# Kernel optimization log

Hardware: AMD Instinct MI355X
Metric: run time of the kernel (lower is better)

The kernel has to match this reference:

```python
import jax, jax.numpy as jnp
import numpy as np

NEG_SLOPE_ATT = 0.2   # GATConv internal leaky_relu slope
NEG_SLOPE_ACT = 0.01  # f.leaky_relu default
LN_EPS = 1e-5

N_NODES, N_EDGES, F_IN = 50000, 400000, 256
HEADS, C1, C2, N_CLS = 4, 256, 128, 32


def gat_conv(x, src, dst, W, a_src, a_dst, bias, concat):
    """PyG GATConv (self-loops already appended to src/dst)."""
    N = x.shape[0]
    H, C = a_src.shape
    h = (x @ W.T).reshape(N, H, C)                      # [N,H,C]
    s = (h * a_src[None]).sum(-1)                       # [N,H] alpha_src
    d = (h * a_dst[None]).sum(-1)                       # [N,H] alpha_dst
    e = jax.nn.leaky_relu(s[src] + d[dst], NEG_SLOPE_ATT)  # [E,H]
    emax = jax.ops.segment_max(e, dst, num_segments=N)
    emax = jnp.where(jnp.isfinite(emax), emax, 0.0)
    p = jnp.exp(e - emax[dst])
    denom = jax.ops.segment_sum(p, dst, num_segments=N)
    alpha = p / (denom[dst] + 1e-16)                    # segment softmax over dst
    out = jax.ops.segment_sum(alpha[:, :, None] * h[src], dst, num_segments=N)
    out = out.reshape(N, H * C) if concat else out.mean(axis=1)
    return out + bias


def layer_norm(x, g, b):
    mu = x.mean(-1, keepdims=True)
    var = jnp.var(x, axis=-1, keepdims=True)
    return (x - mu) / jnp.sqrt(var + LN_EPS) * g + b


def setup_inputs() -> dict:
    key = jax.random.key(0)
    ks = jax.random.split(key, 24)
    def g(k, shape, scale=0.1):
        return jax.random.normal(k, shape, dtype=jnp.float32) * scale
    inp = {
        "x": g(ks[0], (N_NODES, F_IN), 1.0),
        "edge_src": jax.random.randint(ks[1], (N_EDGES,), 0, N_NODES, dtype=jnp.int32),
        "edge_dst": jax.random.randint(ks[2], (N_EDGES,), 0, N_NODES, dtype=jnp.int32),
        # layer 1: in F_IN -> H*C1 (concat)
        "W1": g(ks[3], (HEADS * C1, F_IN)),
        "a_src1": g(ks[4], (HEADS, C1)), "a_dst1": g(ks[5], (HEADS, C1)),
        "b1": jnp.zeros((HEADS * C1,), jnp.float32),
        "ln1_g": jnp.ones((HEADS * C1,), jnp.float32), "ln1_b": jnp.zeros((HEADS * C1,), jnp.float32),
        # layer 2: in H*C1 -> H*C2 (concat)
        "W2": g(ks[6], (HEADS * C2, HEADS * C1)),
        "a_src2": g(ks[7], (HEADS, C2)), "a_dst2": g(ks[8], (HEADS, C2)),
        "b2": jnp.zeros((HEADS * C2,), jnp.float32),
        "ln2_g": jnp.ones((HEADS * C2,), jnp.float32), "ln2_b": jnp.zeros((HEADS * C2,), jnp.float32),
        # layer 3: in H*C2 -> N_CLS (heads=1, mean/no-concat)
        "W3": g(ks[9], (1 * N_CLS, HEADS * C2)),
        "a_src3": g(ks[10], (1, N_CLS)), "a_dst3": g(ks[11], (1, N_CLS)),
        "b3": jnp.zeros((N_CLS,), jnp.float32),
        "ln3_g": jnp.ones((N_CLS,), jnp.float32), "ln3_b": jnp.zeros((N_CLS,), jnp.float32),
    }
    return inp


def reference(x, edge_src, edge_dst,
              W1, a_src1, a_dst1, b1, ln1_g, ln1_b,
              W2, a_src2, a_dst2, b2, ln2_g, ln2_b,
              W3, a_src3, a_dst3, b3, ln3_g, ln3_b):
    N = x.shape[0]
    loops = jnp.arange(N, dtype=edge_src.dtype)  # GATConv add_self_loops=True
    src = jnp.concatenate([edge_src, loops])
    dst = jnp.concatenate([edge_dst, loops])
    # dropout layers are identity in eval mode
    h = gat_conv(x, src, dst, W1, a_src1, a_dst1, b1, True)
    h = jax.nn.leaky_relu(layer_norm(h, ln1_g, ln1_b), NEG_SLOPE_ACT)
    h = gat_conv(h, src, dst, W2, a_src2, a_dst2, b2, True)
    h = jax.nn.leaky_relu(layer_norm(h, ln2_g, ln2_b), NEG_SLOPE_ACT)
    h = gat_conv(h, src, dst, W3, a_src3, a_dst3, b3, False)
    h = layer_norm(h, ln3_g, ln3_b)
    return jax.nn.log_softmax(h, axis=1)
```

## Files before the change

kernel.cpp:

```cpp
#include <hip/hip_runtime.h>
#include <math.h>


#define NEG_ATT 0.2f
#define NEG_ACT 0.01f

typedef __attribute__((ext_vector_type(8))) short bf16x8;
typedef __attribute__((ext_vector_type(8))) unsigned short u16x8;
typedef __attribute__((ext_vector_type(4))) float f32x4;

__device__ __forceinline__ float bf2f(unsigned short u) {
  union { unsigned int i; float f; } c; c.i = ((unsigned int)u) << 16; return c.f;
}
__device__ __forceinline__ unsigned short f2bf(float f) {
  union { float f; unsigned int i; } c; c.f = f;
  unsigned int r = c.i + 0x7FFFu + ((c.i >> 16) & 1u);
  return (unsigned short)(r >> 16);
}

__global__ void cvt_kernel(const float* __restrict__ in,
                           unsigned short* __restrict__ out, int n8) {
  int i = blockIdx.x * 256 + threadIdx.x;
  if (i >= n8) return;
  float4 v0 = reinterpret_cast<const float4*>(in)[i * 2];
  float4 v1 = reinterpret_cast<const float4*>(in)[i * 2 + 1];
  ushort4 o0 = make_ushort4(f2bf(v0.x), f2bf(v0.y), f2bf(v0.z), f2bf(v0.w));
  ushort4 o1 = make_ushort4(f2bf(v1.x), f2bf(v1.y), f2bf(v1.z), f2bf(v1.w));
  reinterpret_cast<ushort4*>(out)[i * 2] = o0;
  reinterpret_cast<ushort4*>(out)[i * 2 + 1] = o1;
}

__global__ __launch_bounds__(256) void qb_kernel(const float* __restrict__ W1,
    const float* __restrict__ as1, const float* __restrict__ ad1,
    unsigned short* __restrict__ Qb) {
  int r = blockIdx.x;
  int k = threadIdx.x;
  if (r >= 8) { Qb[r * 256 + k] = 0; return; }
  int h = r & 3;
  const float* av = (r >> 2) ? ad1 : as1;
  float acc = 0.f;
#pragma unroll 8
  for (int c = 0; c < 256; c++)
    acc += W1[((size_t)(h * 256 + c)) * 256 + k] * av[h * 256 + c];
  Qb[r * 256 + k] = f2bf(acc);
}

__global__ void hist_kernel(const int* __restrict__ edge_dst,
                            int* __restrict__ cnt, int E, int N) {
  int e = blockIdx.x * 256 + threadIdx.x;
  if (e >= E + N) return;
  int dn = (e < E) ? edge_dst[e] : (e - E);
  atomicAdd(&cnt[dn], 1);
}

__global__ __launch_bounds__(1024) void scan_kernel(const int* __restrict__ cnt,
    int* __restrict__ row_ptr, int* __restrict__ cur, int N) {
  __shared__ int sbuf[1024];
  int tid = threadIdx.x;
  int CH = (N + 1023) / 1024;
  int beg = tid * CH;
  int end = beg + CH; if (end > N) end = N;
  int lsum = 0;
  for (int i = beg; i < end; i++) lsum += cnt[i];
  sbuf[tid] = lsum;
  __syncthreads();
  for (int off = 1; off < 1024; off <<= 1) {
    int v = (tid >= off) ? sbuf[tid - off] : 0;
    __syncthreads();
    sbuf[tid] += v;
    __syncthreads();
  }
  int run = sbuf[tid] - lsum;
  for (int i = beg; i < end; i++) {
    row_ptr[i] = run; cur[i] = run;
    run += cnt[i];
  }
  if (tid == 1023) row_ptr[N] = sbuf[1023];
}

__global__ void scatter_kernel(const int* __restrict__ edge_src,
                               const int* __restrict__ edge_dst,
                               int* __restrict__ cur,
                               int* __restrict__ src_sorted, int E, int N) {
  int e = blockIdx.x * 256 + threadIdx.x;
  if (e >= E + N) return;
  int sn, dn;
  if (e < E) { sn = edge_src[e]; dn = edge_dst[e]; }
  else       { sn = dn = e - E; }
  int pos = atomicAdd(&cur[dn], 1);
  src_sorted[pos] = sn;
}

#define GLOBAL_AS __attribute__((address_space(1)))
#define LDS_AS __attribute__((address_space(3)))

__device__ __forceinline__ void gload_lds16(const void* g, void* l) {
  __builtin_amdgcn_global_load_lds((const GLOBAL_AS unsigned int*)g,
                                   (LDS_AS unsigned int*)l, 16, 0, 0);
}

template <int BM, int BN, int WM, int WN, bool F32OUT>
__global__ __launch_bounds__(256) void gemm_mfma(
    const unsigned short* __restrict__ A, const unsigned short* __restrict__ B,
    void* __restrict__ Cv, const float* __restrict__ bias,
    int M, int N, int K, int lda, int ldb, int ldc,
    long long aZ, long long bZ, long long cZ, int biasZ) {
  constexpr int BK = 64;
  constexpr int FM = BM / (WM * 16);
  constexpr int FN = BN / (WN * 16);
  A += (size_t)blockIdx.z * aZ;
  B += (size_t)blockIdx.z * bZ;
  const size_t cbase = (size_t)blockIdx.z * cZ;
  __shared__ unsigned short As[BM * BK];
  __shared__ unsigned short Bs[BN * BK];
  const int tid = threadIdx.x;
  const int w = tid >> 6, lane = tid & 63;
  const int wm = w / WN, wn = w % WN;
  const int bm = blockIdx.x * BM, bn = blockIdx.y * BN;
  const int l15 = lane & 15, l4 = lane >> 4;

  f32x4 acc[FM][FN] = {};

  constexpr int CHA = BM * BK / 8;
  constexpr int CHB = BN * BK / 8;

  for (int k0 = 0; k0 < K; k0 += BK) {
#pragma unroll
    for (int c0 = 0; c0 < CHA; c0 += 256) {
      int c = c0 + tid;
      if (CHA - c0 >= 256 || tid < CHA - c0) {
        int cl = c ^ ((c >> 3) & 7);
        int row = cl >> 3;
        int kk = (cl & 7) * 8;
        int gr = bm + row; if (gr > M - 1) gr = M - 1;
        gload_lds16(A + (size_t)gr * lda + k0 + kk,
                    As + (size_t)(c0 + (tid & ~63)) * 8);
      }
    }
#pragma unroll
    for (int c0 = 0; c0 < CHB; c0 += 256) {
      int c = c0 + tid;
      if (CHB - c0 >= 256 || tid < CHB - c0) {
        int cl = c ^ ((c >> 3) & 7);
        int row = cl >> 3;
        int kk = (cl & 7) * 8;
        gload_lds16(B + (size_t)(bn + row) * ldb + k0 + kk,
                    Bs + (size_t)(c0 + (tid & ~63)) * 8);
      }
    }
    __syncthreads();
#pragma unroll
    for (int ks = 0; ks < 2; ks++) {
      bf16x8 af[FM], bfr[FN];
#pragma unroll
      for (int i = 0; i < FM; i++) {
        int row = wm * (FM * 16) + i * 16 + l15;
        int byte = row * (BK * 2) + ks * 64 + l4 * 16;
        byte ^= ((byte >> 7) & 7) << 4;
        af[i] = *reinterpret_cast<const bf16x8*>((const char*)As + byte);
      }
#pragma unroll
      for (int i = 0; i < FN; i++) {
        int row = wn * (FN * 16) + i * 16 + l15;
        int byte = row * (BK * 2) + ks * 64 + l4 * 16;
        byte ^= ((byte >> 7) & 7) << 4;
        bfr[i] = *reinterpret_cast<const bf16x8*>((const char*)Bs + byte);
      }
#pragma unroll
      for (int i = 0; i < FM; i++)
#pragma unroll
        for (int jn = 0; jn < FN; jn++)
          acc[i][jn] = __builtin_amdgcn_mfma_f32_16x16x32_bf16(
              af[i], bfr[jn], acc[i][jn], 0, 0, 0);
    }
    __syncthreads();
  }
#pragma unroll
  for (int i = 0; i < FM; i++) {
#pragma unroll
    for (int jn = 0; jn < FN; jn++) {
      int col = bn + wn * (FN * 16) + jn * 16 + l15;
      float bv = bias ? bias[biasZ * blockIdx.z + col] : 0.f;
#pragma unroll
      for (int r = 0; r < 4; r++) {
        int m = bm + wm * (FM * 16) + i * 16 + l4 * 4 + r;
        if (m < M) {
          float val = acc[i][jn][r] + bv;
          if constexpr (F32OUT)
            ((float*)Cv)[cbase + (size_t)m * ldc + col] = val;
          else
            ((unsigned short*)Cv)[cbase + (size_t)m * ldc + col] = f2bf(val);
        }
      }
    }
  }
}

__global__ __launch_bounds__(256) void aggx_kernel(
    const int* __restrict__ row_ptr, const int* __restrict__ src_sorted,
    const float* __restrict__ sd1, const unsigned short* __restrict__ xb,
    unsigned short* __restrict__ y, int N) {
  __shared__ float alds[4][2][64][4];
  int w = threadIdx.x >> 6, lane = threadIdx.x & 63;
  int n = blockIdx.x * 4 + w;
  if (n >= N) return;
  int beg = row_ptr[n], end = row_ptr[n + 1];
  float4 dv = *reinterpret_cast<const float4*>(sd1 + (size_t)n * 16 + 4);

  auto compE = [&](int t, float e[4]) {
    if (t < end) {
      int sj = src_sorted[t];
      float4 sv = *reinterpret_cast<const float4*>(sd1 + (size_t)sj * 16);
      e[0] = sv.x + dv.x; e[1] = sv.y + dv.y;
      e[2] = sv.z + dv.z; e[3] = sv.w + dv.w;
#pragma unroll
      for (int h = 0; h < 4; h++) e[h] = e[h] > 0.f ? e[h] : NEG_ATT * e[h];
    } else {
      e[0] = e[1] = e[2] = e[3] = -1e30f;
    }
  };

  float mx[4] = {-1e30f, -1e30f, -1e30f, -1e30f};
  for (int cb = beg; cb < end; cb += 64) {
    float e[4]; compE(cb + lane, e);
#pragma unroll
    for (int h = 0; h < 4; h++) {
      float m = e[h];
#pragma unroll
      for (int o = 32; o; o >>= 1) m = fmaxf(m, __shfl_xor(m, o));
      mx[h] = fmaxf(mx[h], m);
    }
  }
  float den[4] = {0.f, 0.f, 0.f, 0.f};
  for (int cb = beg; cb < end; cb += 64) {
    float e[4]; compE(cb + lane, e);
#pragma unroll
    for (int h = 0; h < 4; h++) {
      float p = __expf(e[h] - mx[h]);
#pragma unroll
      for (int o = 32; o; o >>= 1) p += __shfl_xor(p, o);
      den[h] += p;
    }
  }
  float ia[4];
#pragma unroll
  for (int h = 0; h < 4; h++) ia[h] = 1.0f / (den[h] + 1e-16f);

  float acc[4][4] = {};
  for (int cb = beg; cb < end; cb += 64) {
    float e[4]; compE(cb + lane, e);
    int pb = ((cb - beg) >> 6) & 1;
    float4 al;
    al.x = __expf(e[0] - mx[0]) * ia[0];
    al.y = __expf(e[1] - mx[1]) * ia[1];
    al.z = __expf(e[2] - mx[2]) * ia[2];
    al.w = __expf(e[3] - mx[3]) * ia[3];
    *reinterpret_cast<float4*>(alds[w][pb][lane]) = al;
    int cd = end - cb; if (cd > 64) cd = 64;
    for (int j = 0; j < cd; j++) {
      float4 a4 = *reinterpret_cast<const float4*>(alds[w][pb][j]);
      int sj = src_sorted[cb + j];
      ushort4 xv = *reinterpret_cast<const ushort4*>(
          xb + (size_t)sj * 256 + lane * 4);
      float x0 = bf2f(xv.x), x1 = bf2f(xv.y), x2 = bf2f(xv.z), x3 = bf2f(xv.w);
      float ar[4] = {a4.x, a4.y, a4.z, a4.w};
#pragma unroll
      for (int h = 0; h < 4; h++) {
        acc[h][0] = fmaf(ar[h], x0, acc[h][0]);
        acc[h][1] = fmaf(ar[h], x1, acc[h][1]);
        acc[h][2] = fmaf(ar[h], x2, acc[h][2]);
        acc[h][3] = fmaf(ar[h], x3, acc[h][3]);
      }
    }
  }
#pragma unroll
  for (int h = 0; h < 4; h++) {
    ushort4 o = make_ushort4(f2bf(acc[h][0]), f2bf(acc[h][1]),
                             f2bf(acc[h][2]), f2bf(acc[h][3]));
    *reinterpret_cast<ushort4*>(y + (size_t)n * 1024 + h * 256 + lane * 4) = o;
  }
}

__global__ __launch_bounds__(256) void agg2m_kernel(
    const int* __restrict__ row_ptr, const int* __restrict__ src_sorted,
    const float* __restrict__ s2, const float* __restrict__ d2,
    const unsigned short* __restrict__ h2, const float* __restrict__ bias,
    const float* __restrict__ ln_g, const float* __restrict__ ln_b,
    unsigned short* __restrict__ outb, int N) {
  __shared__ float alds[4][2][64][4];
  int w = threadIdx.x >> 6, lane = threadIdx.x & 63;
  int n = blockIdx.x * 4 + w;
  if (n >= N) return;
  int beg = row_ptr[n], end = row_ptr[n + 1];
  int head = lane >> 4, c0 = lane * 8;
  float4 dv = *reinterpret_cast<const float4*>(d2 + (size_t)n * 4);

  auto compE = [&](int t, float e[4]) {
    if (t < end) {
      int sj = src_sorted[t];
      float4 sv = *reinterpret_cast<const float4*>(s2 + (size_t)sj * 4);
      e[0] = sv.x + dv.x; e[1] = sv.y + dv.y;
      e[2] = sv.z + dv.z; e[3] = sv.w + dv.w;
#pragma unroll
      for (int h = 0; h < 4; h++) e[h] = e[h] > 0.f ? e[h] : NEG_ATT * e[h];
    } else {
      e[0] = e[1] = e[2] = e[3] = -1e30f;
    }
  };

  float mx[4] = {-1e30f, -1e30f, -1e30f, -1e30f};
  for (int cb = beg; cb < end; cb += 64) {
    float e[4]; compE(cb + lane, e);
#pragma unroll
    for (int h = 0; h < 4; h++) {
      float m = e[h];
#pragma unroll
      for (int o = 32; o; o >>= 1) m = fmaxf(m, __shfl_xor(m, o));
      mx[h] = fmaxf(mx[h], m);
    }
  }
  float den[4] = {0.f, 0.f, 0.f, 0.f};
  for (int cb = beg; cb < end; cb += 64) {
    float e[4]; compE(cb + lane, e);
#pragma unroll
    for (int h = 0; h < 4; h++) {
      float p = __expf(e[h] - mx[h]);
#pragma unroll
      for (int o = 32; o; o >>= 1) p += __shfl_xor(p, o);
      den[h] += p;
    }
  }
  float ia[4];
#pragma unroll
  for (int h = 0; h < 4; h++) ia[h] = 1.0f / (den[h] + 1e-16f);

  float acc[8] = {};
  for (int cb = beg; cb < end; cb += 64) {
    float e[4]; compE(cb + lane, e);
    int pb = ((cb - beg) >> 6) & 1;
    float4 al;
    al.x = __expf(e[0] - mx[0]) * ia[0];
    al.y = __expf(e[1] - mx[1]) * ia[1];
    al.z = __expf(e[2] - mx[2]) * ia[2];
    al.w = __expf(e[3] - mx[3]) * ia[3];
    *reinterpret_cast<float4*>(alds[w][pb][lane]) = al;
    int cd = end - cb; if (cd > 64) cd = 64;
    for (int j = 0; j < cd; j++) {
      float a = alds[w][pb][j][head];
      int sj = src_sorted[cb + j];
      u16x8 xv = *reinterpret_cast<const u16x8*>(h2 + (size_t)sj * 512 + c0);
#pragma unroll
      for (int i = 0; i < 8; i++)
        acc[i] = fmaf(a, bf2f(xv[i]), acc[i]);
    }
  }
  float v[8], s1 = 0.f, sq = 0.f;
#pragma unroll
  for (int i = 0; i < 8; i++) {
    v[i] = acc[i] + bias[c0 + i];
    s1 += v[i]; sq += v[i] * v[i];
  }
#pragma unroll
  for (int o = 32; o; o >>= 1) { s1 += __shfl_xor(s1, o); sq += __shfl_xor(sq, o); }
  float mean = s1 * (1.0f / 512.0f);
  float var = sq * (1.0f / 512.0f) - mean * mean;
  float rstd = rsqrtf(var + 1e-5f);
  u16x8 ov;
#pragma unroll
  for (int i = 0; i < 8; i++) {
    float yv = (v[i] - mean) * rstd * ln_g[c0 + i] + ln_b[c0 + i];
    yv = yv > 0.f ? yv : NEG_ACT * yv;
    ov[i] = f2bf(yv);
  }
  *reinterpret_cast<u16x8*>(outb + (size_t)n * 512 + c0) = ov;
}

__global__ __launch_bounds__(256) void ln1024_kernel(
    const unsigned short* __restrict__ z, const float* __restrict__ ln_g,
    const float* __restrict__ ln_b, unsigned short* __restrict__ outb, int N) {
  int n = blockIdx.x;
  int tid = threadIdx.x;
  int c0 = tid * 4;
  ushort4 zv = *reinterpret_cast<const ushort4*>(z + (size_t)n * 1024 + c0);
  float v[4] = {bf2f(zv.x), bf2f(zv.y), bf2f(zv.z), bf2f(zv.w)};
  float s1 = v[0] + v[1] + v[2] + v[3];
  float sq = v[0]*v[0] + v[1]*v[1] + v[2]*v[2] + v[3]*v[3];
#pragma unroll
  for (int o = 32; o; o >>= 1) { s1 += __shfl_down(s1, o); sq += __shfl_down(sq, o); }
  __shared__ float r1[4], r2[4];
  int wave = tid >> 6, lane = tid & 63;
  if (lane == 0) { r1[wave] = s1; r2[wave] = sq; }
  __syncthreads();
  float t1 = r1[0] + r1[1] + r1[2] + r1[3];
  float t2 = r2[0] + r2[1] + r2[2] + r2[3];
  float mean = t1 * (1.0f / 1024.0f);
  float var = t2 * (1.0f / 1024.0f) - mean * mean;
  float rstd = rsqrtf(var + 1e-5f);
  ushort4 ov;
  float y0 = (v[0] - mean) * rstd * ln_g[c0 + 0] + ln_b[c0 + 0];
  float y1 = (v[1] - mean) * rstd * ln_g[c0 + 1] + ln_b[c0 + 1];
  float y2 = (v[2] - mean) * rstd * ln_g[c0 + 2] + ln_b[c0 + 2];
  float y3 = (v[3] - mean) * rstd * ln_g[c0 + 3] + ln_b[c0 + 3];
  ov.x = f2bf(y0 > 0.f ? y0 : NEG_ACT * y0);
  ov.y = f2bf(y1 > 0.f ? y1 : NEG_ACT * y1);
  ov.z = f2bf(y2 > 0.f ? y2 : NEG_ACT * y2);
  ov.w = f2bf(y3 > 0.f ? y3 : NEG_ACT * y3);
  *reinterpret_cast<ushort4*>(outb + (size_t)n * 1024 + c0) = ov;
}

__global__ __launch_bounds__(256) void sd128_kernel(
    const unsigned short* __restrict__ h, const float* __restrict__ a_src,
    const float* __restrict__ a_dst, float* __restrict__ s,
    float* __restrict__ d, int N) {
  int n = blockIdx.x;
  int head = threadIdx.x >> 6;
  int lane = threadIdx.x & 63;
  const unsigned short* row = h + (size_t)n * 512 + head * 128 + lane * 2;
  ushort2 u = *reinterpret_cast<const ushort2*>(row);
  float2 a = *reinterpret_cast<const float2*>(a_src + head * 128 + lane * 2);
  float2 b = *reinterpret_cast<const float2*>(a_dst + head * 128 + lane * 2);
  float ss = bf2f(u.x) * a.x + bf2f(u.y) * a.y;
  float dd = bf2f(u.x) * b.x + bf2f(u.y) * b.y;
#pragma unroll
  for (int o = 32; o; o >>= 1) { ss += __shfl_down(ss, o); dd += __shfl_down(dd, o); }
  if (lane == 0) { s[(size_t)n * 4 + head] = ss; d[(size_t)n * 4 + head] = dd; }
}

__global__ __launch_bounds__(256) void sd32_kernel(
    const unsigned short* __restrict__ h, const float* __restrict__ a_src,
    const float* __restrict__ a_dst, float* __restrict__ s,
    float* __restrict__ d, int N) {
  int idx = blockIdx.x * 256 + threadIdx.x;
  int n = idx >> 5, c = idx & 31;
  if (n >= N) return;
  float v = bf2f(h[(size_t)n * 32 + c]);
  float ss = v * a_src[c], dd = v * a_dst[c];
#pragma unroll
  for (int o = 16; o; o >>= 1) { ss += __shfl_xor(ss, o, 32); dd += __shfl_xor(dd, o, 32); }
  if (c == 0) { s[n] = ss; d[n] = dd; }
}

__global__ void stats_kernel(const int* __restrict__ row_ptr,
    const int* __restrict__ src_sorted, const float* __restrict__ s,
    const float* __restrict__ d, float* __restrict__ p_sorted,
    float* __restrict__ inv_den, int N) {
  int idx = blockIdx.x * blockDim.x + threadIdx.x;
  if (idx >= N) return;
  int n = idx;
  int beg = row_ptr[n], end = row_ptr[n + 1];
  float dn = d[n];
  float mx = -1e30f;
  for (int j = beg; j < end; j++) {
    float v = s[src_sorted[j]] + dn;
    v = v > 0.f ? v : NEG_ATT * v;
    mx = fmaxf(mx, v);
  }
  float den = 0.f;
  for (int j = beg; j < end; j++) {
    float v = s[src_sorted[j]] + dn;
    v = v > 0.f ? v : NEG_ATT * v;
    float p = __expf(v - mx);
    p_sorted[j] = p;
    den += p;
  }
  inv_den[n] = 1.0f / (den + 1e-16f);
}

__global__ __launch_bounds__(256) void final_kernel(
    const int* __restrict__ row_ptr, const int* __restrict__ src_sorted,
    const float* __restrict__ p_sorted, const float* __restrict__ inv_den,
    const unsigned short* __restrict__ h3, const float* __restrict__ b3,
    const float* __restrict__ g3, const float* __restrict__ bb3,
    float* __restrict__ out, int N) {
  int idx = blockIdx.x * 256 + threadIdx.x;
  int n = idx >> 5, c = idx & 31;
  if (n >= N) return;
  int beg = row_ptr[n], end = row_ptr[n + 1];
  float acc = 0.f;
  for (int j = beg; j < end; j++)
    acc = fmaf(p_sorted[j], bf2f(h3[(size_t)src_sorted[j] * 32 + c]), acc);
  float v = acc * inv_den[n] + b3[c];
  float s1 = v, s2 = v * v;
#pragma unroll
  for (int o = 16; o; o >>= 1) { s1 += __shfl_xor(s1, o, 32); s2 += __shfl_xor(s2, o, 32); }
  float mean = s1 * (1.f / 32.f), var = s2 * (1.f / 32.f) - mean * mean;
  float y = (v - mean) * rsqrtf(var + 1e-5f) * g3[c] + bb3[c];
  float mx = y;
#pragma unroll
  for (int o = 16; o; o >>= 1) mx = fmaxf(mx, __shfl_xor(mx, o, 32));
  float ex = __expf(y - mx), se = ex;
#pragma unroll
  for (int o = 16; o; o >>= 1) se += __shfl_xor(se, o, 32);
  out[(size_t)n * 32 + c] = y - mx - __logf(se);
}

extern "C" void kernel_launch(void* const* d_in, const int* in_sizes, int n_in,
                              void* d_out, int out_size, void* d_ws,
                              size_t ws_size, hipStream_t stream) {
  const float* x   = (const float*)d_in[0];
  const int* esrc  = (const int*)d_in[1];
  const int* edst  = (const int*)d_in[2];
  const float* W1  = (const float*)d_in[3];
  const float* as1 = (const float*)d_in[4];
  const float* ad1 = (const float*)d_in[5];
  const float* b1  = (const float*)d_in[6];
  const float* g1  = (const float*)d_in[7];
  const float* bb1 = (const float*)d_in[8];
  const float* W2  = (const float*)d_in[9];
  const float* as2 = (const float*)d_in[10];
  const float* ad2 = (const float*)d_in[11];
  const float* b2  = (const float*)d_in[12];
  const float* g2  = (const float*)d_in[13];
  const float* bb2 = (const float*)d_in[14];
  const float* W3  = (const float*)d_in[15];
  const float* as3 = (const float*)d_in[16];
  const float* ad3 = (const float*)d_in[17];
  const float* b3  = (const float*)d_in[18];
  const float* g3  = (const float*)d_in[19];
  const float* bb3 = (const float*)d_in[20];
  float* out = (float*)d_out;

  const int Nn = in_sizes[0] / 256;
  const int E  = in_sizes[1];
  const int Etot = E + Nn;

  char* ws = (char*)d_ws;
  size_t off = 0;
  auto alloc = [&](size_t bytes) -> char* {
    char* p = ws + off;
    off += (bytes + 255) & ~(size_t)255;
    return p;
  };
  int* cnt        = (int*)alloc((size_t)(Nn + 1) * 4);
  int* cur        = (int*)alloc((size_t)(Nn + 1) * 4);
  int* row_ptr    = (int*)alloc((size_t)(Nn + 1) * 4);
  int* src_sorted = (int*)alloc((size_t)Etot * 4);
  float* sd1   = (float*)alloc((size_t)Nn * 16 * 4);
  float* s2    = (float*)alloc((size_t)Nn * 4 * 4);
  float* d2    = (float*)alloc((size_t)Nn * 4 * 4);
  float* s3    = (float*)alloc((size_t)Nn * 4);
  float* d3    = (float*)alloc((size_t)Nn * 4);
  float* invd3 = (float*)alloc((size_t)Nn * 4);
  float* p3    = (float*)alloc((size_t)Etot * 4);
  unsigned short* W1b = (unsigned short*)alloc((size_t)1024 * 256 * 2);
  unsigned short* W2b = (unsigned short*)alloc((size_t)512 * 1024 * 2);
  unsigned short* W3b = (unsigned short*)alloc((size_t)32 * 512 * 2);
  unsigned short* Qb  = (unsigned short*)alloc((size_t)16 * 256 * 2);
  unsigned short* h3  = (unsigned short*)alloc((size_t)Nn * 32 * 2);
  unsigned short* regA = (unsigned short*)alloc((size_t)Nn * 1024 * 2);
  unsigned short* regB = (unsigned short*)alloc((size_t)Nn * 1024 * 2);
  unsigned short* y    = regA;
  unsigned short* act1 = regA;
  unsigned short* act2 = regA;
  unsigned short* xb   = regB;
  unsigned short* z1   = regB;
  unsigned short* h2   = regB;

  const int mb = (Nn + 127) / 128;

  cvt_kernel<<<(Nn * 256 / 8 + 255) / 256, 256, 0, stream>>>(x, xb, Nn * 256 / 8);
  cvt_kernel<<<(1024 * 256 / 8 + 255) / 256, 256, 0, stream>>>(W1, W1b, 1024 * 256 / 8);
  cvt_kernel<<<(512 * 1024 / 8 + 255) / 256, 256, 0, stream>>>(W2, W2b, 512 * 1024 / 8);
  cvt_kernel<<<(32 * 512 / 8 + 255) / 256, 256, 0, stream>>>(W3, W3b, 32 * 512 / 8);
  qb_kernel<<<16, 256, 0, stream>>>(W1, as1, ad1, Qb);

  hipMemsetAsync(cnt, 0, (size_t)(Nn + 1) * 4, stream);
  int eb = (Etot + 255) / 256;
  hist_kernel<<<eb, 256, 0, stream>>>(edst, cnt, E, Nn);
  scan_kernel<<<1, 1024, 0, stream>>>(cnt, row_ptr, cur, Nn);
  scatter_kernel<<<eb, 256, 0, stream>>>(esrc, edst, cur, src_sorted, E, Nn);

  gemm_mfma<128, 16, 4, 1, true><<<dim3(mb, 1, 1), 256, 0, stream>>>(
      xb, Qb, sd1, nullptr, Nn, 16, 256, 256, 256, 16, 0, 0, 0, 0);
  aggx_kernel<<<(Nn + 3) / 4, 256, 0, stream>>>(row_ptr, src_sorted, sd1, xb, y, Nn);
  gemm_mfma<128, 128, 2, 2, false><<<dim3(mb, 2, 4), 256, 0, stream>>>(
      y, W1b, z1, b1, Nn, 256, 256, 1024, 256, 1024, 256LL, 256LL * 256, 256LL, 256);
  ln1024_kernel<<<Nn, 256, 0, stream>>>(z1, g1, bb1, act1, Nn);

  gemm_mfma<128, 128, 2, 2, false><<<dim3(mb, 4, 1), 256, 0, stream>>>(
      act1, W2b, h2, nullptr, Nn, 512, 1024, 1024, 1024, 512, 0, 0, 0, 0);
  sd128_kernel<<<Nn, 256, 0, stream>>>(h2, as2, ad2, s2, d2, Nn);
  agg2m_kernel<<<(Nn + 3) / 4, 256, 0, stream>>>(row_ptr, src_sorted, s2, d2,
                                                 h2, b2, g2, bb2, act2, Nn);

  gemm_mfma<128, 32, 4, 1, false><<<dim3(mb, 1, 1), 256, 0, stream>>>(
      act2, W3b, h3, nullptr, Nn, 32, 512, 512, 512, 32, 0, 0, 0, 0);
  sd32_kernel<<<(Nn * 32 + 255) / 256, 256, 0, stream>>>(h3, as3, ad3, s3, d3, Nn);
  stats_kernel<<<(Nn + 255) / 256, 256, 0, stream>>>(row_ptr, src_sorted,
                                                     s3, d3, p3, invd3, Nn);
  final_kernel<<<(Nn * 32 + 255) / 256, 256, 0, stream>>>(row_ptr, src_sorted,
      p3, invd3, h3, b3, g3, bb3, out, Nn);
}
```

Measured before the change: 781.7 us.

## Parallelize CSR prefix scan across blocks and swap GEMM grid order for A reuse

Replaces the single-block 1024-thread serial-chunk prefix scan over node degrees with a three-kernel block scan (per-block sums, scan of block sums, per-block local scan plus offset). This removes the long serial per-thread loops in the old one-block scan. Separately, adds a SWAPXY template option so the large layer-1 and layer-2 GEMMs launch with N-tiles on blockIdx.x, letting consecutive blocks share the same A row-tile in cache. The scan handles at most 256 blocks, which limits it to 65536 nodes, and it adds two extra launches.

```diff
diff --git a/kernel.cpp b/kernel.cpp
--- a/kernel.cpp
+++ b/kernel.cpp
@@ -53,29 +53,61 @@
   atomicAdd(&cnt[dn], 1);
 }
 
-__global__ __launch_bounds__(1024) void scan_kernel(const int* __restrict__ cnt,
+__global__ __launch_bounds__(256) void scan1_kernel(
+    const int* __restrict__ cnt, int* __restrict__ bsum, int N) {
+  __shared__ int sd_[256];
+  int i = blockIdx.x * 256 + threadIdx.x;
+  int v = (i < N) ? cnt[i] : 0;
+  sd_[threadIdx.x] = v;
+  __syncthreads();
+#pragma unroll
+  for (int off = 128; off; off >>= 1) {
+    if (threadIdx.x < off) sd_[threadIdx.x] += sd_[threadIdx.x + off];
+    __syncthreads();
+  }
+  if (threadIdx.x == 0) bsum[blockIdx.x] = sd_[0];
+}
+
+__global__ __launch_bounds__(256) void scan2_kernel(
+    const int* __restrict__ bsum, int* __restrict__ boff,
+    int* __restrict__ row_ptr, int NB, int N) {
+  __shared__ int sd_[256];
+  int t = threadIdx.x;
+  int v = (t < NB) ? bsum[t] : 0;
+  sd_[t] = v;
+  __syncthreads();
+#pragma unroll
+  for (int off = 1; off < 256; off <<= 1) {
+    int u = (t >= off) ? sd_[t - off] : 0;
+    __syncthreads();
+    sd_[t] += u;
+    __syncthreads();
+  }
+  if (t < NB) boff[t] = sd_[t] - v;
+  if (t == 255) row_ptr[N] = sd_[255];
+}
+
+__global__ __launch_bounds__(256) void scan3_kernel(
+    const int* __restrict__ cnt, const int* __restrict__ boff,
     int* __restrict__ row_ptr, int* __restrict__ cur, int N) {
-  __shared__ int sbuf[1024];
-  int tid = threadIdx.x;
-  int CH = (N + 1023) / 1024;
-  int beg = tid * CH;
-  int end = beg + CH; if (end > N) end = N;
-  int lsum = 0;
-  for (int i = beg; i < end; i++) lsum += cnt[i];
-  sbuf[tid] = lsum;
+  __shared__ int sd_[256];
+  int t = threadIdx.x;
+  int i = blockIdx.x * 256 + t;
+  int v = (i < N) ? cnt[i] : 0;
+  sd_[t] = v;
   __syncthreads();
-  for (int off = 1; off < 1024; off <<= 1) {
-    int v = (tid >= off) ? sbuf[tid - off] : 0;
+#pragma unroll
+  for (int off = 1; off < 256; off <<= 1) {
+    int u = (t >= off) ? sd_[t - off] : 0;
     __syncthreads();
-    sbuf[tid] += v;
+    sd_[t] += u;
     __syncthreads();
   }
-  int run = sbuf[tid] - lsum;
-  for (int i = beg; i < end; i++) {
-    row_ptr[i] = run; cur[i] = run;
-    run += cnt[i];
-  }
-  if (tid == 1023) row_ptr[N] = sbuf[1023];
+  if (i < N) {
+    int val = boff[blockIdx.x] + sd_[t] - v;
+    row_ptr[i] = val;
+    cur[i] = val;
+  }
 }
 
 __global__ void scatter_kernel(const int* __restrict__ edge_src,
@@ -99,7 +131,7 @@
                                    (LDS_AS unsigned int*)l, 16, 0, 0);
 }
 
-template <int BM, int BN, int WM, int WN, bool F32OUT>
+template <int BM, int BN, int WM, int WN, bool F32OUT, bool SWAPXY>
 __global__ __launch_bounds__(256) void gemm_mfma(
     const unsigned short* __restrict__ A, const unsigned short* __restrict__ B,
     void* __restrict__ Cv, const float* __restrict__ bias,
@@ -116,7 +148,8 @@
   const int tid = threadIdx.x;
   const int w = tid >> 6, lane = tid & 63;
   const int wm = w / WN, wn = w % WN;
-  const int bm = blockIdx.x * BM, bn = blockIdx.y * BN;
+  const int bm = (SWAPXY ? blockIdx.y : blockIdx.x) * BM;
+  const int bn = (SWAPXY ? blockIdx.x : blockIdx.y) * BN;
   const int l15 = lane & 15, l4 = lane >> 4;
 
   f32x4 acc[FM][FN] = {};
@@ -523,6 +556,7 @@
   const int Nn = in_sizes[0] / 256;
   const int E  = in_sizes[1];
   const int Etot = E + Nn;
+  const int NB = (Nn + 255) / 256;
 
   char* ws = (char*)d_ws;
   size_t off = 0;
@@ -534,6 +568,8 @@
   int* cnt        = (int*)alloc((size_t)(Nn + 1) * 4);
   int* cur        = (int*)alloc((size_t)(Nn + 1) * 4);
   int* row_ptr    = (int*)alloc((size_t)(Nn + 1) * 4);
+  int* bsum       = (int*)alloc(256 * 4);
+  int* boff       = (int*)alloc(256 * 4);
   int* src_sorted = (int*)alloc((size_t)Etot * 4);
   float* sd1   = (float*)alloc((size_t)Nn * 16 * 4);
   float* s2    = (float*)alloc((size_t)Nn * 4 * 4);
@@ -567,23 +603,25 @@
   hipMemsetAsync(cnt, 0, (size_t)(Nn + 1) * 4, stream);
   int eb = (Etot + 255) / 256;
   hist_kernel<<<eb, 256, 0, stream>>>(edst, cnt, E, Nn);
-  scan_kernel<<<1, 1024, 0, stream>>>(cnt, row_ptr, cur, Nn);
+  scan1_kernel<<<NB, 256, 0, stream>>>(cnt, bsum, Nn);
+  scan2_kernel<<<1, 256, 0, stream>>>(bsum, boff, row_ptr, NB, Nn);
+  scan3_kernel<<<NB, 256, 0, stream>>>(cnt, boff, row_ptr, cur, Nn);
   scatter_kernel<<<eb, 256, 0, stream>>>(esrc, edst, cur, src_sorted, E, Nn);
 
-  gemm_mfma<128, 16, 4, 1, true><<<dim3(mb, 1, 1), 256, 0, stream>>>(
+  gemm_mfma<128, 16, 4, 1, true, false><<<dim3(mb, 1, 1), 256, 0, stream>>>(
       xb, Qb, sd1, nullptr, Nn, 16, 256, 256, 256, 16, 0, 0, 0, 0);
   aggx_kernel<<<(Nn + 3) / 4, 256, 0, stream>>>(row_ptr, src_sorted, sd1, xb, y, Nn);
-  gemm_mfma<128, 128, 2, 2, false><<<dim3(mb, 2, 4), 256, 0, stream>>>(
+  gemm_mfma<128, 128, 2, 2, false, true><<<dim3(2, mb, 4), 256, 0, stream>>>(
       y, W1b, z1, b1, Nn, 256, 256, 1024, 256, 1024, 256LL, 256LL * 256, 256LL, 256);
   ln1024_kernel<<<Nn, 256, 0, stream>>>(z1, g1, bb1, act1, Nn);
 
-  gemm_mfma<128, 128, 2, 2, false><<<dim3(mb, 4, 1), 256, 0, stream>>>(
+  gemm_mfma<128, 128, 2, 2, false, true><<<dim3(4, mb, 1), 256, 0, stream>>>(
       act1, W2b, h2, nullptr, Nn, 512, 1024, 1024, 1024, 512, 0, 0, 0, 0);
   sd128_kernel<<<Nn, 256, 0, stream>>>(h2, as2, ad2, s2, d2, Nn);
   agg2m_kernel<<<(Nn + 3) / 4, 256, 0, stream>>>(row_ptr, src_sorted, s2, d2,
                                                  h2, b2, g2, bb2, act2, Nn);
 
-  gemm_mfma<128, 32, 4, 1, false><<<dim3(mb, 1, 1), 256, 0, stream>>>(
+  gemm_mfma<128, 32, 4, 1, false, false><<<dim3(mb, 1, 1), 256, 0, stream>>>(
       act2, W3b, h3, nullptr, Nn, 32, 512, 512, 512, 32, 0, 0, 0, 0);
   sd32_kernel<<<(Nn * 32 + 255) / 256, 256, 0, stream>>>(h3, as3, ad3, s3, d3, Nn);
   stats_kernel<<<(Nn + 255) / 256, 256, 0, stream>>>(row_ptr, src_sorted,
```

New measurement: 689.6 us. 1.13x faster.
